# Kernel optimization log

Hardware: AMD Instinct MI355X
Metric: run time of the kernel (lower is better)

The kernel has to match this reference:

```python
import math
import jax, jax.numpy as jnp
import numpy as np

B, S, D = 2, 2048, 1024
H, DK = 16, 64
NUM_BUCKETS = 32
MAX_DISTANCE = 128


def _relative_position_bucket(relative_position, num_buckets=NUM_BUCKETS, max_distance=MAX_DISTANCE):
    # bidirectional=True branch (encoder / non-causal)
    n = -relative_position
    num_buckets = num_buckets // 2
    ret = (n < 0).astype(jnp.int32) * num_buckets
    n = jnp.abs(n)
    max_exact = num_buckets // 2
    is_small = n < max_exact
    # guard log(0); masked out by is_small anyway
    n_safe = jnp.maximum(n, 1).astype(jnp.float32)
    val_if_large = max_exact + (
        jnp.log(n_safe / max_exact) / math.log(max_distance / max_exact) * (num_buckets - max_exact)
    ).astype(jnp.int32)
    val_if_large = jnp.minimum(val_if_large, num_buckets - 1)
    return ret + jnp.where(is_small, n, val_if_large)


def setup_inputs() -> dict:
    key = jax.random.key(0)
    ks = jax.random.split(key, 6)
    std_q = (D * DK) ** -0.5
    std = D ** -0.5
    return {
        "x": jax.random.normal(ks[0], (B, S, D), jnp.float32),
        "q_w": jax.random.normal(ks[1], (H * DK, D), jnp.float32) * std_q,
        "k_w": jax.random.normal(ks[2], (H * DK, D), jnp.float32) * std,
        "v_w": jax.random.normal(ks[3], (H * DK, D), jnp.float32) * std,
        "o_w": jax.random.normal(ks[4], (D, H * DK), jnp.float32) * ((H * DK) ** -0.5),
        "rel_bias": jax.random.normal(ks[5], (NUM_BUCKETS, H), jnp.float32) * std,
    }


def reference(x, q_w, k_w, v_w, o_w, rel_bias):
    b, s, _ = x.shape
    # project and split heads: [B, H, S, DK]
    def proj(w):
        return (x @ w.T).reshape(b, s, H, DK).transpose(0, 2, 1, 3)
    q, k, v = proj(q_w), proj(k_w), proj(v_w)

    # T5-style unscaled attention scores: [B, H, Sq, Sk]
    scores = jnp.einsum("bhqd,bhkd->bhqk", q, k)

    # bucketed relative-position bias
    ctx = jnp.arange(s)[:, None]
    mem = jnp.arange(s)[None, :]
    rp_bucket = _relative_position_bucket(mem - ctx)  # [S, S]
    bias = rel_bias[rp_bucket]                        # [S, S, H]
    bias = bias.transpose(2, 0, 1)[None]              # [1, H, S, S]
    scores = scores + bias

    attn = jax.nn.softmax(scores, axis=-1)
    ctx_out = jnp.einsum("bhqk,bhkd->bhqd", attn, v)
    ctx_out = ctx_out.transpose(0, 2, 1, 3).reshape(b, s, H * DK)
    return ctx_out @ o_w.T
```

## Files before the change

kernel.cpp:

```cpp
#include <hip/hip_runtime.h>
#include <stdint.h>


typedef unsigned short u16;
typedef __attribute__((ext_vector_type(8))) short short8;
typedef __attribute__((ext_vector_type(4))) float float4v;
typedef __attribute__((ext_vector_type(4))) u16 ushort4v;
typedef __attribute__((ext_vector_type(4))) uint32_t uint4v;

typedef __attribute__((address_space(1))) void void_g;
typedef __attribute__((address_space(3))) void void_l;

#define L2E 1.4426950408889634f

__device__ __forceinline__ u16 f2b(float f) {
  union { float f; uint32_t u; } v; v.f = f;
  uint32_t r = (v.u + 0x7fffu + ((v.u >> 16) & 1u)) >> 16;
  return (u16)r;
}
__device__ __forceinline__ u16 f2b_fast(float f) {
  union { float f; uint32_t u; } v; v.f = f;
  return (u16)((v.u + 0x8000u) >> 16);
}
__device__ __forceinline__ uint32_t cvt_pk_bf16(float lo, float hi) {
  uint32_t r;
  asm("v_cvt_pk_bf16_f32 %0, %1, %2" : "=v"(r) : "v"(lo), "v"(hi));
  return r;
}

__global__ void cvt_all(const float* __restrict__ x,  const float* __restrict__ qw,
                        const float* __restrict__ kw, const float* __restrict__ vw,
                        const float* __restrict__ ow, const float* __restrict__ rel_bias,
                        u16* __restrict__ xb, u16* __restrict__ wqkv, u16* __restrict__ owb,
                        float* __restrict__ biasT) {
  int bi = blockIdx.x;
  if (bi >= 8192) {
    int idx = (bi - 8192) * 256 + threadIdx.x;
    int h = idx >> 12, t = idx & 4095;
    if (t > 4094) { biasT[h * 4096 + 4095] = -1.0e4f; return; }
    int d = t - 2047;
    int n = -d;
    int ret = (n < 0) ? 16 : 0;
    int na = (n < 0) ? -n : n;
    int bucket;
    if (na < 8) {
      bucket = ret + na;
    } else {
      float v = logf((float)na / 8.0f) / logf(16.0f) * 8.0f;
      int vi = 8 + (int)v;
      bucket = ret + (vi > 15 ? 15 : vi);
    }
    biasT[h * 4096 + t] = (rel_bias[bucket * 16 + h] - 8.0f) * L2E;
    return;
  }
  int i = bi * 256 + threadIdx.x;
  const float* s; u16* d; int off;
  if (i < 1048576)      { s = x;  d = xb;              off = i; }
  else if (i < 1310720) { s = qw; d = wqkv;            off = i - 1048576; }
  else if (i < 1572864) { s = kw; d = wqkv + 1048576;  off = i - 1310720; }
  else if (i < 1835008) { s = vw; d = wqkv + 2097152;  off = i - 1572864; }
  else                  { s = ow; d = owb;             off = i - 1835008; }
  float4v v = ((const float4v*)s)[off];
  ushort4v o;
  o.x = f2b(v.x); o.y = f2b(v.y); o.z = f2b(v.z); o.w = f2b(v.w);
  ((ushort4v*)d)[off] = o;
}

__global__ __launch_bounds__(256, 3)
void gemm_qkv(const u16* __restrict__ A, const u16* __restrict__ W,
              u16* __restrict__ qkb, u16* __restrict__ vTp) {
  const int K = 1024;
  __shared__ __align__(16) char SM[34816];
  u16* As = (u16*)SM;
  u16* Bs = (u16*)(SM + 16384);
  const int tid = threadIdx.x;
  const int wid = tid >> 6;
  const int lane = tid & 63;
  const int row16 = lane & 15, oct = lane >> 4;
  const int lin = blockIdx.x + blockIdx.y * 32;
  const int V = (lin & 7) * 96 + (lin >> 3);
  const int bx = V & 31, by = V >> 5;
  const int tm = bx * 128, tn = by * 128;
  const int wm = (wid & 1) * 64, wn = (wid >> 1) * 64;
  const int srow = lane >> 2;
  const int sc = (lane & 3) * 8;
  float4v acc[4][4] = {};
  for (int k0 = 0; k0 < K; k0 += 64) {
    __syncthreads();
#pragma unroll
    for (int i = 0; i < 4; i++) {
      const int idx = i * 4 + wid;
      const int kk = idx & 1;
      const int rb = idx >> 1;
      const int r = rb * 16 + srow;
      const int c = kk * 32 + sc;
      __builtin_amdgcn_global_load_lds((void_g*)(A + (size_t)(tm + r) * K + k0 + c),
                                       (void_l*)(As + (kk * 128 + rb * 16) * 32), 16, 0, 0);
      __builtin_amdgcn_global_load_lds((void_g*)(W + (size_t)(tn + r) * K + k0 + c),
                                       (void_l*)(Bs + (kk * 128 + rb * 16) * 32), 16, 0, 0);
    }
    __syncthreads();
#pragma unroll
    for (int kk = 0; kk < 2; kk++) {
      short8 af[4], bfr[4];
#pragma unroll
      for (int mi = 0; mi < 4; mi++)
        af[mi] = *(const short8*)(As + (kk * 128 + wm + mi * 16 + row16) * 32 + oct * 8);
#pragma unroll
      for (int ni = 0; ni < 4; ni++)
        bfr[ni] = *(const short8*)(Bs + (kk * 128 + wn + ni * 16 + row16) * 32 + oct * 8);
#pragma unroll
      for (int mi = 0; mi < 4; mi++)
#pragma unroll
        for (int ni = 0; ni < 4; ni++)
          acc[mi][ni] = __builtin_amdgcn_mfma_f32_16x16x32_bf16(af[mi], bfr[ni], acc[mi][ni], 0, 0, 0);
    }
  }

  if (tn < 2048) {
    u16* Es = (u16*)SM;
    __syncthreads();
#pragma unroll
    for (int mi = 0; mi < 4; mi++)
#pragma unroll
      for (int ni = 0; ni < 4; ni++)
#pragma unroll
        for (int r = 0; r < 4; r++)
          Es[(wm + mi * 16 + oct * 4 + r) * 136 + wn + ni * 16 + row16] = f2b(acc[mi][ni][r]);
    __syncthreads();
#pragma unroll
    for (int it = 0; it < 8; it++) {
      int idx = it * 256 + tid;
      int row = idx >> 4, c = idx & 15;
      short8 v = *(const short8*)(Es + row * 136 + c * 8);
      *(short8*)(qkb + (size_t)(tm + row) * 2048 + tn + c * 8) = v;
    }
  } else {
    const int h0 = (tn - 2048) >> 6;
    const int b = tm >> 11;
    const int s0 = tm & 2047;
#pragma unroll
    for (int ni = 0; ni < 4; ni++) {
      const int dg = wn + ni * 16 + row16;
      const int head = h0 + (dg >> 6), d = dg & 63;
      u16* vdst = vTp + ((size_t)((b * 16 + head) * 64 + d)) * 2048 + s0 + wm + oct * 8;
#pragma unroll
      for (int bb = 0; bb < 2; bb++) {
        uint4v pw;
        pw.x = cvt_pk_bf16(acc[2 * bb][ni][0], acc[2 * bb][ni][1]);
        pw.y = cvt_pk_bf16(acc[2 * bb][ni][2], acc[2 * bb][ni][3]);
        pw.z = cvt_pk_bf16(acc[2 * bb + 1][ni][0], acc[2 * bb + 1][ni][1]);
        pw.w = cvt_pk_bf16(acc[2 * bb + 1][ni][2], acc[2 * bb + 1][ni][3]);
        *(uint4v*)(vdst + bb * 32) = pw;
      }
    }
  }
}

__global__ __launch_bounds__(256, 2)
void gemm_out(const u16* __restrict__ A, const u16* __restrict__ W,
              float* __restrict__ C) {
  const int K = 1024, N = 1024;
  __shared__ __align__(16) char SM[49152];
  const int tid = threadIdx.x;
  const int wid = tid >> 6;
  const int lane = tid & 63;
  const int row16 = lane & 15, oct = lane >> 4;
  const int tm = blockIdx.x * 64, tn = blockIdx.y * 128;
  const int wm = (wid & 1) * 32, wn = (wid >> 1) * 64;
  const int srow = lane >> 2;
  const int sc = (lane & 3) * 8;
  float4v acc[2][4] = {};

#define STAGE_OUT(buf, k0)                                                            \
  {                                                                                   \
    u16* Ad = (u16*)(SM + (buf) * 24576);                                             \
    u16* Bd = (u16*)(SM + (buf) * 24576 + 8192);                                      \
    _Pragma("unroll")                                                                 \
    for (int i = 0; i < 2; i++) {                                                     \
      const int idx = i * 4 + wid;                                                    \
      const int kk = idx & 1;                                                         \
      const int rb = idx >> 1;                                                        \
      const int r = rb * 16 + srow;                                                   \
      const int c = kk * 32 + sc;                                                     \
      __builtin_amdgcn_global_load_lds((void_g*)(A + (size_t)(tm + r) * K + (k0) + c),\
                                       (void_l*)(Ad + (kk * 64 + rb * 16) * 32), 16, 0, 0); \
    }                                                                                 \
    _Pragma("unroll")                                                                 \
    for (int i = 0; i < 4; i++) {                                                     \
      const int idx = i * 4 + wid;                                                    \
      const int kk = idx & 1;                                                         \
      const int rb = idx >> 1;                                                        \
      const int r = rb * 16 + srow;                                                   \
      const int c = kk * 32 + sc;                                                     \
      __builtin_amdgcn_global_load_lds((void_g*)(W + (size_t)(tn + r) * K + (k0) + c),\
                                       (void_l*)(Bd + (kk * 128 + rb * 16) * 32), 16, 0, 0); \
    }                                                                                 \
  }

  STAGE_OUT(0, 0);
  __syncthreads();
  for (int t = 0; t < 16; t++) {
    if (t + 1 < 16) STAGE_OUT((t + 1) & 1, (t + 1) * 64);
    const u16* As = (const u16*)(SM + (t & 1) * 24576);
    const u16* Bs = As + 4096;
#pragma unroll
    for (int kk = 0; kk < 2; kk++) {
      short8 af[2], bfr[4];
#pragma unroll
      for (int mi = 0; mi < 2; mi++)
        af[mi] = *(const short8*)(As + (kk * 64 + wm + mi * 16 + row16) * 32 + oct * 8);
#pragma unroll
      for (int ni = 0; ni < 4; ni++)
        bfr[ni] = *(const short8*)(Bs + (kk * 128 + wn + ni * 16 + row16) * 32 + oct * 8);
#pragma unroll
      for (int mi = 0; mi < 2; mi++)
#pragma unroll
        for (int ni = 0; ni < 4; ni++)
          acc[mi][ni] = __builtin_amdgcn_mfma_f32_16x16x32_bf16(af[mi], bfr[ni], acc[mi][ni], 0, 0, 0);
    }
    __syncthreads();
  }
#pragma unroll
  for (int mi = 0; mi < 2; mi++)
#pragma unroll
    for (int ni = 0; ni < 4; ni++)
#pragma unroll
      for (int r = 0; r < 4; r++)
        C[(size_t)(tm + wm + mi * 16 + oct * 4 + r) * N + tn + wn + ni * 16 + row16] =
            acc[mi][ni][r];
}

__global__ __launch_bounds__(256, 2)
void flash_attn(const u16* __restrict__ qkb, const u16* __restrict__ vTp,
                const float* __restrict__ biasT, u16* __restrict__ ctx) {
  const int S = 2048, LDQ = 2048;
  const int lin = blockIdx.x + (blockIdx.y << 4) + (blockIdx.z << 8);
  const int V = (lin & 7) * 64 + (lin >> 3);
  const int qt0 = (V & 15) * 128;
  const int h = (V >> 4) & 15, b = V >> 8;
  const int tid = threadIdx.x, wid = tid >> 6, lane = tid & 63;
  const int row16 = lane & 15, oct = lane >> 4;

  __shared__ __align__(16) float biasS[2176];
  __shared__ __align__(16) u16 Ks[2][2][64][40];
  __shared__ __align__(16) u16 Vts[2][2][64][40];

  {
    const float* bsrc = biasT + h * 4096 + (1920 - qt0);
    for (int i = tid; i < 544; i += 256)
      ((float4v*)biasS)[i] = ((const float4v*)bsrc)[i];
  }
  const float bias_neg = biasT[h * 4096];
  const float bias_pos = biasT[h * 4096 + 4094];

  const u16* qbase = qkb + ((size_t)b * S + qt0 + wid * 32) * LDQ + h * 64;
  short8 qf[2][2];
#pragma unroll
  for (int f = 0; f < 2; f++)
#pragma unroll
    for (int hd = 0; hd < 2; hd++)
      qf[f][hd] = *(const short8*)(qbase + (size_t)(f * 16 + row16) * LDQ + hd * 32 + oct * 8);

  float4v l_acc[2] = {};
  float4v o_acc[2][4] = {};
  const short8 ones = {0x3F80, 0x3F80, 0x3F80, 0x3F80, 0x3F80, 0x3F80, 0x3F80, 0x3F80};

  const int sr = lane >> 2, c8 = (lane & 3) * 8;
  const int srow = wid * 16 + sr;
  const u16* Kst = qkb + 1024 + ((size_t)b * S + srow) * LDQ + c8 + h * 64;
  const u16* Vst = vTp + ((size_t)(b * 16 + h) * 64 + srow) * 2048 + c8;

  short8 kreg[2], vreg[2];
#pragma unroll
  for (int hd = 0; hd < 2; hd++) kreg[hd] = *(const short8*)(Kst + hd * 32);
#pragma unroll
  for (int ks = 0; ks < 2; ks++) vreg[ks] = *(const short8*)(Vst + ks * 32);
#pragma unroll
  for (int hd = 0; hd < 2; hd++) *(short8*)&Ks[0][hd][srow][c8] = kreg[hd];
#pragma unroll
  for (int ks = 0; ks < 2; ks++) *(short8*)&Vts[0][ks][srow][c8] = vreg[ks];
#pragma unroll
  for (int hd = 0; hd < 2; hd++) kreg[hd] = *(const short8*)(Kst + (size_t)64 * LDQ + hd * 32);
#pragma unroll
  for (int ks = 0; ks < 2; ks++) vreg[ks] = *(const short8*)(Vst + 64 + ks * 32);
  __syncthreads();

  for (int kt = 0; kt < S; kt += 64) {
    const int cur = (kt >> 6) & 1, nb = cur ^ 1;
    if (kt + 64 < S) {
#pragma unroll
      for (int hd = 0; hd < 2; hd++) *(short8*)&Ks[nb][hd][srow][c8] = kreg[hd];
#pragma unroll
      for (int ks = 0; ks < 2; ks++) *(short8*)&Vts[nb][ks][srow][c8] = vreg[ks];
    }
    if (kt + 128 < S) {
#pragma unroll
      for (int hd = 0; hd < 2; hd++)
        kreg[hd] = *(const short8*)(Kst + (size_t)(kt + 128) * LDQ + hd * 32);
#pragma unroll
      for (int ks = 0; ks < 2; ks++)
        vreg[ks] = *(const short8*)(Vst + (kt + 128) + ks * 32);
    }

    short8 kf[4][2];
#pragma unroll
    for (int st = 0; st < 4; st++)
#pragma unroll
      for (int hd = 0; hd < 2; hd++)
        kf[st][hd] = *(const short8*)&Ks[cur][hd][st * 16 + row16][oct * 8];

    float4v sc[2][4];
#pragma unroll
    for (int f = 0; f < 2; f++)
#pragma unroll
      for (int st = 0; st < 4; st++) {
        float4v s = {};
        s = __builtin_amdgcn_mfma_f32_16x16x32_bf16(kf[st][0], qf[f][0], s, 0, 0, 0);
        s = __builtin_amdgcn_mfma_f32_16x16x32_bf16(kf[st][1], qf[f][1], s, 0, 0, 0);
        sc[f][st] = s;
      }

    short8 vf[2][4];
#pragma unroll
    for (int ks = 0; ks < 2; ks++)
#pragma unroll
      for (int ni = 0; ni < 4; ni++)
        vf[ks][ni] = *(const short8*)&Vts[cur][ks][ni * 16 + row16][oct * 8];

    const int dk = kt - qt0;
    const bool far = (dk >= 256) || (dk <= -192);
    if (far) {
      const float bc = (dk > 0) ? bias_pos : bias_neg;
#pragma unroll
      for (int f = 0; f < 2; f++)
#pragma unroll
        for (int st = 0; st < 4; st++)
#pragma unroll
          for (int r = 0; r < 4; r++)
            sc[f][st][r] = __builtin_amdgcn_exp2f(__builtin_fmaf(sc[f][st][r], L2E, bc));
    } else {
#pragma unroll
      for (int f = 0; f < 2; f++) {
        const int basef = kt + oct * 4 - wid * 32 - f * 16 - row16 + 127;
#pragma unroll
        for (int st = 0; st < 4; st++)
#pragma unroll
          for (int r = 0; r < 4; r++)
            sc[f][st][r] = __builtin_amdgcn_exp2f(
                __builtin_fmaf(sc[f][st][r], L2E, biasS[basef + st * 16 + r]));
      }
    }

#pragma unroll
    for (int f = 0; f < 2; f++) {
#pragma unroll
      for (int ks = 0; ks < 2; ks++) {
        uint4v pw;
        pw.x = cvt_pk_bf16(sc[f][2 * ks][0], sc[f][2 * ks][1]);
        pw.y = cvt_pk_bf16(sc[f][2 * ks][2], sc[f][2 * ks][3]);
        pw.z = cvt_pk_bf16(sc[f][2 * ks + 1][0], sc[f][2 * ks + 1][1]);
        pw.w = cvt_pk_bf16(sc[f][2 * ks + 1][2], sc[f][2 * ks + 1][3]);
        short8 pf = __builtin_bit_cast(short8, pw);
#pragma unroll
        for (int ni = 0; ni < 4; ni++)
          o_acc[f][ni] = __builtin_amdgcn_mfma_f32_16x16x32_bf16(pf, vf[ks][ni], o_acc[f][ni], 0, 0, 0);
        l_acc[f] = __builtin_amdgcn_mfma_f32_16x16x32_bf16(pf, ones, l_acc[f], 0, 0, 0);
      }
    }
    asm volatile("s_waitcnt lgkmcnt(0)" ::: "memory");
    __builtin_amdgcn_s_barrier();
    __builtin_amdgcn_sched_barrier(0);
  }

#pragma unroll
  for (int f = 0; f < 2; f++) {
    float linv[4];
#pragma unroll
    for (int r = 0; r < 4; r++)
      linv[r] = 1.0f / l_acc[f][r];
    const size_t orow = (size_t)b * S + qt0 + wid * 32 + f * 16 + oct * 4;
#pragma unroll
    for (int ni = 0; ni < 4; ni++)
#pragma unroll
      for (int r = 0; r < 4; r++)
        ctx[(orow + r) * 1024 + h * 64 + ni * 16 + row16] = f2b_fast(o_acc[f][ni][r] * linv[r]);
  }
}

extern "C" void kernel_launch(void* const* d_in, const int* in_sizes, int n_in,
                              void* d_out, int out_size, void* d_ws, size_t ws_size,
                              hipStream_t stream) {
  const float* x        = (const float*)d_in[0];
  const float* q_w      = (const float*)d_in[1];
  const float* k_w      = (const float*)d_in[2];
  const float* v_w      = (const float*)d_in[3];
  const float* o_w      = (const float*)d_in[4];
  const float* rel_bias = (const float*)d_in[5];

  char* ws = (char*)d_ws;
  u16*   xb    = (u16*)(ws);
  u16*   wqkv  = (u16*)(ws + 8388608);
  u16*   owb   = (u16*)(ws + 14680064);
  u16*   qkb   = (u16*)(ws + 16777216);
  u16*   vTp   = (u16*)(ws + 33554432);
  u16*   ctxb  = (u16*)(ws + 41943040);
  float* biasT = (float*)(ws + 50331648);

  cvt_all<<<8448, 256, 0, stream>>>(x, q_w, k_w, v_w, o_w, rel_bias,
                                    xb, wqkv, owb, biasT);

  dim3 g1(4096 / 128, 3072 / 128);
  gemm_qkv<<<g1, 256, 0, stream>>>(xb, wqkv, qkb, vTp);

  dim3 g2(2048 / 128, 16, 2);
  flash_attn<<<g2, 256, 0, stream>>>(qkb, vTp, biasT, ctxb);

  dim3 g3(4096 / 64, 1024 / 128);
  gemm_out<<<g3, 256, 0, stream>>>(ctxb, owb, (float*)d_out);
}
```

Baseline: 172.5 us.

## Load K and V fragments directly from global memory, dropping LDS staging

Removes the double-buffered shared-memory staging of K and V tiles, together with the per-iteration barrier. Each wave now reads its MFMA fragments straight from global memory, relying on L2/L1 caching for reuse across the four waves. This removes the LDS write/read traffic and block-wide synchronisation. In exchange each wave issues four times the global loads, there is no explicit prefetch to hide latency, and the loads are less coalesced.

```diff
diff --git a/kernel.cpp b/kernel.cpp
--- a/kernel.cpp
+++ b/kernel.cpp
@@ -243,8 +243,6 @@
   const int row16 = lane & 15, oct = lane >> 4;
 
   __shared__ __align__(16) float biasS[2176];
-  __shared__ __align__(16) u16 Ks[2][2][64][40];
-  __shared__ __align__(16) u16 Vts[2][2][64][40];
 
   {
     const float* bsrc = biasT + h * 4096 + (1920 - qt0);
@@ -266,49 +264,18 @@
   float4v o_acc[2][4] = {};
   const short8 ones = {0x3F80, 0x3F80, 0x3F80, 0x3F80, 0x3F80, 0x3F80, 0x3F80, 0x3F80};
 
-  const int sr = lane >> 2, c8 = (lane & 3) * 8;
-  const int srow = wid * 16 + sr;
-  const u16* Kst = qkb + 1024 + ((size_t)b * S + srow) * LDQ + c8 + h * 64;
-  const u16* Vst = vTp + ((size_t)(b * 16 + h) * 64 + srow) * 2048 + c8;
-
-  short8 kreg[2], vreg[2];
-#pragma unroll
-  for (int hd = 0; hd < 2; hd++) kreg[hd] = *(const short8*)(Kst + hd * 32);
-#pragma unroll
-  for (int ks = 0; ks < 2; ks++) vreg[ks] = *(const short8*)(Vst + ks * 32);
-#pragma unroll
-  for (int hd = 0; hd < 2; hd++) *(short8*)&Ks[0][hd][srow][c8] = kreg[hd];
-#pragma unroll
-  for (int ks = 0; ks < 2; ks++) *(short8*)&Vts[0][ks][srow][c8] = vreg[ks];
-#pragma unroll
-  for (int hd = 0; hd < 2; hd++) kreg[hd] = *(const short8*)(Kst + (size_t)64 * LDQ + hd * 32);
-#pragma unroll
-  for (int ks = 0; ks < 2; ks++) vreg[ks] = *(const short8*)(Vst + 64 + ks * 32);
+  const u16* Kbase = qkb + 1024 + ((size_t)b * S + row16) * LDQ + h * 64 + oct * 8;
+  const u16* Vbase = vTp + ((size_t)(b * 16 + h) * 64 + row16) * 2048 + oct * 8;
+
   __syncthreads();
 
   for (int kt = 0; kt < S; kt += 64) {
-    const int cur = (kt >> 6) & 1, nb = cur ^ 1;
-    if (kt + 64 < S) {
-#pragma unroll
-      for (int hd = 0; hd < 2; hd++) *(short8*)&Ks[nb][hd][srow][c8] = kreg[hd];
-#pragma unroll
-      for (int ks = 0; ks < 2; ks++) *(short8*)&Vts[nb][ks][srow][c8] = vreg[ks];
-    }
-    if (kt + 128 < S) {
+    short8 kf[4][2];
+#pragma unroll
+    for (int st = 0; st < 4; st++)
 #pragma unroll
       for (int hd = 0; hd < 2; hd++)
-        kreg[hd] = *(const short8*)(Kst + (size_t)(kt + 128) * LDQ + hd * 32);
-#pragma unroll
-      for (int ks = 0; ks < 2; ks++)
-        vreg[ks] = *(const short8*)(Vst + (kt + 128) + ks * 32);
-    }
-
-    short8 kf[4][2];
-#pragma unroll
-    for (int st = 0; st < 4; st++)
-#pragma unroll
-      for (int hd = 0; hd < 2; hd++)
-        kf[st][hd] = *(const short8*)&Ks[cur][hd][st * 16 + row16][oct * 8];
+        kf[st][hd] = *(const short8*)(Kbase + (size_t)(kt + st * 16) * LDQ + hd * 32);
 
     float4v sc[2][4];
 #pragma unroll
@@ -326,7 +293,7 @@
     for (int ks = 0; ks < 2; ks++)
 #pragma unroll
       for (int ni = 0; ni < 4; ni++)
-        vf[ks][ni] = *(const short8*)&Vts[cur][ks][ni * 16 + row16][oct * 8];
+        vf[ks][ni] = *(const short8*)(Vbase + (size_t)(ni * 16) * 2048 + kt + ks * 32);
 
     const int dk = kt - qt0;
     const bool far = (dk >= 256) || (dk <= -192);
@@ -368,9 +335,6 @@
         l_acc[f] = __builtin_amdgcn_mfma_f32_16x16x32_bf16(pf, ones, l_acc[f], 0, 0, 0);
       }
     }
-    asm volatile("s_waitcnt lgkmcnt(0)" ::: "memory");
-    __builtin_amdgcn_s_barrier();
-    __builtin_amdgcn_sched_barrier(0);
   }
 
 #pragma unroll
```

Measured after the change: 243.6 us. +41.2%, slower.
